# Kernel optimization log

Hardware: AMD Instinct MI355X
Metric: run time of the kernel (lower is better)

## Reference

```python
import jax, jax.numpy as jnp
import numpy as np

EPS = 1e-5
B, C, T = 128, 64, 1000          # batch, EEG channels, time samples
NCLU, HID, NOUT = 8, 512, 4      # clusters, head hidden dim, outputs (=feature_dim)


def _conv1d(x, w):
    # x: (N, Cin, T), w: (Cout, Cin, K), valid conv along time
    return jax.lax.conv_general_dilated(x, w, (1,), 'VALID',
                                        dimension_numbers=('NCH', 'OIH', 'NCH'))


def _bn(x, g, b, m, v):
    # eval-mode BatchNorm over channel dim of (N, C, T)
    return (x - m[None, :, None]) * (g / jnp.sqrt(v + EPS))[None, :, None] + b[None, :, None]


def _pool3(x):
    # maxpool kernel 3 stride 3 along time
    return jax.lax.reduce_window(x, -jnp.inf, jax.lax.max, (1, 1, 3), (1, 1, 3), 'VALID')


def setup_inputs() -> dict:
    key = jax.random.key(0)
    ks = jax.random.split(key, 12)
    def nrm(k, shape, fan):
        return jax.random.normal(k, shape, jnp.float32) / np.float32(np.sqrt(fan))
    inp = {
        'x': jax.random.normal(ks[0], (B, C, T), jnp.float32),
        'cluster_ids': jax.random.randint(ks[1], (B,), 0, NCLU, jnp.int32),
        # Deep4Net-style backbone params
        'w_time': nrm(ks[2], (25, 1, 10), 10),
        'b_time': jnp.zeros((25,), jnp.float32),
        'w_spat': nrm(ks[3], (25, 25, C), 25 * C),
        'w2': nrm(ks[4], (50, 25, 10), 250),
        'w3': nrm(ks[5], (100, 50, 10), 500),
        'w4': nrm(ks[6], (200, 100, 10), 1000),
        'w_cls': nrm(ks[7], (NOUT, 200, 7), 1400),
        'b_cls': jnp.zeros((NOUT,), jnp.float32),
        # per-cluster expert head params
        'hW1': nrm(ks[8], (NCLU, HID, NOUT), NOUT),
        'hb1': jnp.zeros((NCLU, HID), jnp.float32),
        'hW2': nrm(ks[9], (NCLU, NOUT, HID), HID),
        'hb2': jnp.zeros((NCLU, NOUT), jnp.float32),
        'hg': jnp.ones((NCLU, HID), jnp.float32),
        'hbe': jnp.zeros((NCLU, HID), jnp.float32),
        'hm': jnp.zeros((NCLU, HID), jnp.float32),
        'hv': jnp.ones((NCLU, HID), jnp.float32),
    }
    for i, c in zip((1, 2, 3, 4), (25, 50, 100, 200)):
        inp[f'g{i}'] = jnp.ones((c,), jnp.float32)
        inp[f'be{i}'] = jnp.zeros((c,), jnp.float32)
        inp[f'm{i}'] = jnp.zeros((c,), jnp.float32)
        inp[f'v{i}'] = jnp.ones((c,), jnp.float32)
    return inp


def reference(x, cluster_ids, w_time, b_time, w_spat, w2, w3, w4, w_cls, b_cls,
              hW1, hb1, hW2, hb2, hg, hbe, hm, hv,
              g1, be1, m1, v1, g2, be2, m2, v2, g3, be3, m3, v3, g4, be4, m4, v4):
    b_, c_, t_ = x.shape
    # conv_time: same 25 temporal filters applied per EEG channel -> (B, C, 25, T1)
    h = _conv1d(x.reshape(b_ * c_, 1, t_), w_time) + b_time[None, :, None]
    h = h.reshape(b_, c_, 25, -1)
    # conv_spat: collapse EEG channel axis -> (B, 25, T1)
    z = jnp.einsum('bcft,gfc->bgt', h, w_spat)
    z = _pool3(jax.nn.elu(_bn(z, g1, be1, m1, v1)))
    for w, g, be, m, v in ((w2, g2, be2, m2, v2), (w3, g3, be3, m3, v3), (w4, g4, be4, m4, v4)):
        z = _pool3(jax.nn.elu(_bn(_conv1d(z, w), g, be, m, v)))
    # final_conv_length='auto': classifier conv reduces time dim to 1 -> (B, NOUT)
    feats = (_conv1d(z, w_cls) + b_cls[None, :, None])[:, :, 0]
    # per-sample expert head routing (Linear -> BN(eval) -> ReLU -> [Dropout eval] -> Linear)
    h1 = jnp.einsum('bf,bhf->bh', feats, hW1[cluster_ids]) + hb1[cluster_ids]
    h1 = (h1 - hm[cluster_ids]) * (hg[cluster_ids] / jnp.sqrt(hv[cluster_ids] + EPS)) + hbe[cluster_ids]
    h1 = jax.nn.relu(h1)
    return jnp.einsum('bh,boh->bo', h1, hW2[cluster_ids]) + hb2[cluster_ids]
```

## Files before the change

kernel.cpp:

```cpp
#include <hip/hip_runtime.h>
#include <math.h>

#define EPS_BN 1e-5f

typedef __attribute__((ext_vector_type(8))) short short8;
typedef __attribute__((ext_vector_type(4))) float f32x4;
typedef __attribute__((ext_vector_type(4))) unsigned int uint4v;

__device__ __forceinline__ unsigned short f2bf(float f) {
    unsigned int u = __float_as_uint(f);
    u = (u + 0x7fffu + ((u >> 16) & 1u)) >> 16;
    return (unsigned short)u;
}
__device__ __forceinline__ float bf2f(unsigned short s) {
    return __uint_as_float(((unsigned int)s) << 16);
}
__device__ __forceinline__ float elu1(float y) { return y > 0.f ? y : expm1f(y); }
__device__ __forceinline__ float warp_sum(float v) {
    for (int off = 32; off > 0; off >>= 1) v += __shfl_down(v, off);
    return v;
}

#define UW1 0
#define UW2 20480
#define UW3 40960
#define UW4 122880
#define BB1 0
#define BB2 32
#define BB3 96
#define BB4 224
#define XTG_U 410496
#define Z1G_U 9192320
#define Z2G_U 10544000
#define Z3G_U 11420544
#define Z4G_BYTE 24372992

#define NPREP 1602
#define RS_ZB 36

__global__ __launch_bounds__(256) void kprep_tr(
    const float* __restrict__ x,
    const float* __restrict__ w_time, const float* __restrict__ b_time,
    const float* __restrict__ w_spat,
    const float* __restrict__ w2, const float* __restrict__ w3,
    const float* __restrict__ w4,
    const float* __restrict__ g1, const float* __restrict__ be1,
    const float* __restrict__ m1, const float* __restrict__ v1,
    const float* __restrict__ g2, const float* __restrict__ be2,
    const float* __restrict__ m2, const float* __restrict__ v2,
    const float* __restrict__ g3, const float* __restrict__ be3,
    const float* __restrict__ m3, const float* __restrict__ v3,
    const float* __restrict__ g4, const float* __restrict__ be4,
    const float* __restrict__ m4, const float* __restrict__ v4,
    unsigned short* __restrict__ wsz, float* __restrict__ biasf) {
    __shared__ float tr[64 * 65];
    if (blockIdx.x < NPREP) {
        int idx = blockIdx.x * 256 + threadIdx.x;
        if (idx < 20480) {
            int k = idx >> 11, g = (idx >> 6) & 31, c = idx & 63;
            float val = 0.f;
            if (g < 25) {
                float s = 0.f;
#pragma unroll
                for (int f = 0; f < 25; ++f)
                    s = fmaf(w_spat[g * 1600 + f * 64 + c], w_time[f * 10 + k], s);
                val = s * (g1[g] * rsqrtf(v1[g] + EPS_BN));
            }
            wsz[UW1 + idx] = f2bf(val);
        } else if (idx < 40960) {
            int j = idx - 20480;
            int k = j >> 11, g = (j >> 5) & 63, c = j & 31;
            float val = 0.f;
            if (g < 50 && c < 25)
                val = w2[(g * 25 + c) * 10 + k] * (g2[g] * rsqrtf(v2[g] + EPS_BN));
            wsz[UW2 + j] = f2bf(val);
        } else if (idx < 122880) {
            int j = idx - 40960;
            int k = j >> 13, g = (j >> 6) & 127, c = j & 63;
            float val = 0.f;
            if (g < 100 && c < 50)
                val = w3[(g * 50 + c) * 10 + k] * (g3[g] * rsqrtf(v3[g] + EPS_BN));
            wsz[UW3 + j] = f2bf(val);
        } else if (idx < 409600) {
            int j = idx - 122880;
            int k = j / 28672, r = j % 28672, g = r >> 7, c = r & 127;
            float val = 0.f;
            if (g < 200 && c < 100)
                val = w4[(g * 100 + c) * 10 + k] * (g4[g] * rsqrtf(v4[g] + EPS_BN));
            wsz[UW4 + j] = f2bf(val);
        } else if (idx < 410048) {
            int j = idx - 409600;
            if (j < 32) {
                int g = j; float val = 0.f;
                if (g < 25) {
                    float beff = 0.f;
                    for (int f = 0; f < 25; ++f) {
                        float a = 0.f;
                        for (int c = 0; c < 64; ++c) a += w_spat[g * 1600 + f * 64 + c];
                        beff = fmaf(a, b_time[f], beff);
                    }
                    float sc = g1[g] * rsqrtf(v1[g] + EPS_BN);
                    val = be1[g] - m1[g] * sc + beff * sc;
                }
                biasf[BB1 + g] = val;
            } else if (j < 96) {
                int g = j - 32; float val = 0.f;
                if (g < 50) { float sc = g2[g] * rsqrtf(v2[g] + EPS_BN); val = be2[g] - m2[g] * sc; }
                biasf[BB2 + g] = val;
            } else if (j < 224) {
                int g = j - 96; float val = 0.f;
                if (g < 100) { float sc = g3[g] * rsqrtf(v3[g] + EPS_BN); val = be3[g] - m3[g] * sc; }
                biasf[BB3 + g] = val;
            } else {
                int g = j - 224; float val = 0.f;
                if (g < 200) { float sc = g4[g] * rsqrtf(v4[g] + EPS_BN); val = be4[g] - m4[g] * sc; }
                biasf[BB4 + g] = val;
            }
        }
    } else {
        const int bid = blockIdx.x - NPREP;
        const int b = bid / 17, tile = bid % 17, t = threadIdx.x;
        const int t0 = tile * 64;
        const float* xb = x + b * 64000;
        for (int idx = t; idx < 1024; idx += 256) {
            int c = idx >> 4, q = idx & 15;
            int tg = t0 + 4 * q;
            float4 v = {0.f, 0.f, 0.f, 0.f};
            if (tg + 4 <= 1000) {
                v = *(const float4*)(xb + c * 1000 + tg);
            } else {
                float* pv = (float*)&v;
#pragma unroll
                for (int e = 0; e < 4; ++e)
                    if (tg + e < 1000) pv[e] = xb[c * 1000 + tg + e];
            }
            tr[c * 65 + 4 * q]     = v.x;
            tr[c * 65 + 4 * q + 1] = v.y;
            tr[c * 65 + 4 * q + 2] = v.z;
            tr[c * 65 + 4 * q + 3] = v.w;
        }
        __syncthreads();
        unsigned short* xTg = wsz + XTG_U;
        for (int idx = t; idx < 2048; idx += 256) {
            int tl = idx >> 5, cp = idx & 31;
            int tg = t0 + tl;
            unsigned int pk = 0u;
            if (tg < 1000)
                pk = (unsigned int)f2bf(tr[(2 * cp) * 65 + tl]) |
                     ((unsigned int)f2bf(tr[(2 * cp + 1) * 65 + tl]) << 16);
            if (tg < 1072)
                *(unsigned int*)&xTg[(b * 1072 + tg) * 64 + 2 * cp] = pk;
        }
    }
}

template<int CPAD, int RS, int SP, int TT, int TPC, int NCHUNK, int JMAX,
         int NTCH, int GPAD, int TPOOL, int GSTORE, int NGV, int OUT_RS,
         bool OUT_F32, int NW, int KPRE>
__device__ __forceinline__ void conv_core(
    const unsigned short* xT, const unsigned short* __restrict__ wpk,
    const float* __restrict__ bias,
    unsigned short* zout, float* zoutf, unsigned short* zb,
    int t, int jbeg, int jend, int t0b) {
    const int lane = t & 63;
    const int wv = __builtin_amdgcn_readfirstlane(t >> 6);
    const int lm = lane & 15, h8 = lane >> 4;
    const int gloc = lane & 31, hh = lane >> 5;
    unsigned short* zbw = zb + wv * (48 * RS_ZB);

    for (int job = jbeg + wv; job < jend; job += NW) {
        const int gbi = job / NTCH, tci = job % NTCH;
        const int tl0 = tci * (TT * 16) - t0b;
        const int po0 = tci * (NCHUNK * 16);

        f32x4 acc[TT][2];
#pragma unroll
        for (int i = 0; i < TT; ++i) {
            acc[i][0] = (f32x4){0.f, 0.f, 0.f, 0.f};
            acc[i][1] = (f32x4){0.f, 0.f, 0.f, 0.f};
        }

        const int abase = (tl0 + lm) * RS + h8 * 8;
        const unsigned short* wp = wpk + (gbi * 32 + lm) * CPAD + h8 * 8;
#pragma unroll
        for (int ph = 0; ph < 10 / KPRE; ++ph) {
            short8 w0r[KPRE][SP], w1r[KPRE][SP];
#pragma unroll
            for (int kk = 0; kk < KPRE; ++kk) {
                const int k = ph * KPRE + kk;
#pragma unroll
                for (int s = 0; s < SP; ++s) {
                    w0r[kk][s] = *(const short8*)(wp + k * (GPAD * CPAD) + s * 32);
                    w1r[kk][s] = *(const short8*)(wp + k * (GPAD * CPAD) + 16 * CPAD + s * 32);
                }
            }
#pragma unroll
            for (int kk = 0; kk < KPRE; ++kk) {
                const int k = ph * KPRE + kk;
#pragma unroll
                for (int s = 0; s < SP; ++s) {
#pragma unroll
                    for (int tt = 0; tt < TT; ++tt) {
                        short8 a = *(const short8*)&xT[abase + (tt * 16 + k) * RS + s * 32];
                        acc[tt][0] = __builtin_amdgcn_mfma_f32_16x16x32_bf16(
                            a, w0r[kk][s], acc[tt][0], 0, 0, 0);
                        acc[tt][1] = __builtin_amdgcn_mfma_f32_16x16x32_bf16(
                            a, w1r[kk][s], acc[tt][1], 0, 0, 0);
                    }
                }
            }
        }

        const float bv0 = bias[gbi * 32 + lm];
        const float bv1 = bias[gbi * 32 + 16 + lm];
#pragma unroll
        for (int ch = 0; ch < NCHUNK; ++ch) {
#pragma unroll
            for (int ti = 0; ti < TPC; ++ti) {
                int ttg = ch * TPC + ti;
#pragma unroll
                for (int r = 0; r < 4; ++r) {
                    float v0 = elu1(acc[ttg][0][r] + bv0);
                    float v1 = elu1(acc[ttg][1][r] + bv1);
                    int row = ti * 16 + 4 * h8 + r;
                    zbw[row * RS_ZB + lm] = f2bf(v0);
                    zbw[row * RS_ZB + 16 + lm] = f2bf(v1);
                }
            }
#pragma unroll
            for (int j = 0; j < JMAX; ++j) {
                int po = hh + 2 * j;
                if (3 * po + 2 < TPC * 16) {
                    float q0 = bf2f(zbw[(3 * po) * RS_ZB + gloc]);
                    float q1 = bf2f(zbw[(3 * po + 1) * RS_ZB + gloc]);
                    float q2 = bf2f(zbw[(3 * po + 2) * RS_ZB + gloc]);
                    float mx = fmaxf(q0, fmaxf(q1, q2));
                    int poa = po0 + ch * 16 + po;
                    int ga = gbi * 32 + gloc;
                    if (poa < TPOOL && ga < GSTORE) {
                        if constexpr (OUT_F32)
                            zoutf[poa * OUT_RS + ga] = mx;
                        else
                            zout[poa * OUT_RS + ga] =
                                (ga < NGV) ? f2bf(mx) : (unsigned short)0;
                    }
                }
            }
        }
    }
}

__global__ __launch_bounds__(64) void ks1(
    const unsigned short* __restrict__ wsu, const float* __restrict__ biasf,
    unsigned short* __restrict__ wsz) {
    __shared__ __align__(16) unsigned short xT[64 * 72];
    __shared__ __align__(16) unsigned short zb[48 * RS_ZB];
    const int b = blockIdx.x, tci = blockIdx.y, t = threadIdx.x;
    const int t0b = tci * 48;
    const unsigned short* xTg = wsz + XTG_U + (b * 1072 + t0b) * 64;
    for (int idx = t; idx < 64 * 8; idx += 64) {
        int r = idx >> 3, q = idx & 7;
        *(uint4v*)&xT[r * 72 + 8 * q] = *(const uint4v*)&xTg[r * 64 + 8 * q];
    }
    __syncthreads();
    conv_core<64, 72, 2, 3, 3, 1, 8, 21, 32, 330, 32, 25, 32, false, 1, 5>(
        xT, wsu + UW1, biasf + BB1, wsz + Z1G_U + b * 330 * 32, nullptr, zb,
        t, tci, tci + 1, t0b);
}

__global__ __launch_bounds__(64) void ks2(
    const unsigned short* __restrict__ wsu, const float* __restrict__ biasf,
    unsigned short* __restrict__ wsz) {
    __shared__ __align__(16) unsigned short xT[64 * 40];
    __shared__ __align__(16) unsigned short zb[48 * RS_ZB];
    const int b = blockIdx.x, job = blockIdx.y, t = threadIdx.x;
    const int t0b = (job % 7) * 48;
    const unsigned short* z1g = wsz + Z1G_U + b * 330 * 32;
    for (int idx = t; idx < 64 * 4; idx += 64) {
        int r = idx >> 2, q = idx & 3;
        uint4v v = {0u, 0u, 0u, 0u};
        if (t0b + r < 330) v = *(const uint4v*)&z1g[(t0b + r) * 32 + 8 * q];
        *(uint4v*)&xT[r * 40 + 8 * q] = v;
    }
    __syncthreads();
    conv_core<32, 40, 1, 3, 3, 1, 8, 7, 64, 107, 64, 50, 64, false, 1, 5>(
        xT, wsu + UW2, biasf + BB2, wsz + Z2G_U + b * 107 * 64, nullptr, zb,
        t, job, job + 1, t0b);
}

__global__ __launch_bounds__(64) void ks3(
    const unsigned short* __restrict__ wsu, const float* __restrict__ biasf,
    unsigned short* __restrict__ wsz) {
    __shared__ __align__(16) unsigned short z2t[64 * 72];
    __shared__ __align__(16) unsigned short zb[48 * RS_ZB];
    const int b = blockIdx.x, job = blockIdx.y, t = threadIdx.x;
    const int t0b = (job % 2) * 48;
    const unsigned short* z2g = wsz + Z2G_U + b * 107 * 64;
    for (int idx = t; idx < 64 * 8; idx += 64) {
        int r = idx >> 3, q = idx & 7;
        uint4v v = {0u, 0u, 0u, 0u};
        if (t0b + r < 107) v = *(const uint4v*)&z2g[(t0b + r) * 64 + 8 * q];
        *(uint4v*)&z2t[r * 72 + 8 * q] = v;
    }
    __syncthreads();
    conv_core<64, 72, 2, 3, 3, 1, 8, 2, 128, 32, 128, 100, 136, false, 1, 5>(
        z2t, wsu + UW3, biasf + BB3, wsz + Z3G_U + b * 44 * 136, nullptr, zb,
        t, job, job + 1, t0b);
}

__global__ __launch_bounds__(64) void ks4(
    const unsigned short* __restrict__ wsu, const float* __restrict__ biasf,
    unsigned short* __restrict__ wsz, float* __restrict__ z4g) {
    __shared__ __align__(16) unsigned short z3t[44 * 136];
    __shared__ __align__(16) unsigned short zb[48 * RS_ZB];
    const int b = blockIdx.x, gbi = blockIdx.y, t = threadIdx.x;
    const unsigned short* z3g = wsz + Z3G_U + b * 44 * 136;
    for (int idx = t; idx < 44 * 17; idx += 64) {
        int r = idx / 17, q = idx % 17;
        uint4v v = {0u, 0u, 0u, 0u};
        if (r < 32) v = *(const uint4v*)&z3g[r * 136 + 8 * q];
        *(uint4v*)&z3t[r * 136 + 8 * q] = v;
    }
    __syncthreads();
    conv_core<128, 136, 4, 2, 2, 1, 4, 1, 224, 7, 200, 200, 200, true, 1, 5>(
        z3t, wsu + UW4, biasf + BB4, nullptr, z4g + b * 1400, zb,
        t, gbi, gbi + 1, 0);
}

__global__ __launch_bounds__(256) void kh(
    const float* __restrict__ z4g,
    const float* __restrict__ w_cls, const float* __restrict__ b_cls,
    const int* __restrict__ cid,
    const float* __restrict__ hW1, const float* __restrict__ hb1,
    const float* __restrict__ hW2, const float* __restrict__ hb2,
    const float* __restrict__ hg, const float* __restrict__ hbe,
    const float* __restrict__ hm, const float* __restrict__ hv,
    float* __restrict__ out) {
    __shared__ float z4f[1400];
    __shared__ float feats[4];
    __shared__ float h1s[512];
    const int b = blockIdx.x, t = threadIdx.x;
    for (int i = t; i < 1400; i += 256) z4f[i] = z4g[b * 1400 + i];
    __syncthreads();

    const int wv = t >> 6, lane = t & 63;
    {
        float p = 0.f;
        for (int i = lane; i < 1400; i += 64) {
            int po = i / 200, g = i - po * 200;
            p = fmaf(z4f[i], w_cls[wv * 1400 + g * 7 + po], p);
        }
        p = warp_sum(p);
        if (lane == 0) feats[wv] = p + b_cls[wv];
    }
    __syncthreads();

    const int c = cid[b];
    const float f0 = feats[0], f1 = feats[1], f2 = feats[2], f3 = feats[3];
    for (int h = t; h < 512; h += 256) {
        const float* w1 = &hW1[(c * 512 + h) * 4];
        float v = f0 * w1[0] + f1 * w1[1] + f2 * w1[2] + f3 * w1[3] + hb1[c * 512 + h];
        float sc = hg[c * 512 + h] * rsqrtf(hv[c * 512 + h] + EPS_BN);
        v = (v - hm[c * 512 + h]) * sc + hbe[c * 512 + h];
        h1s[h] = fmaxf(v, 0.f);
    }
    __syncthreads();
    {
        float p = 0.f;
        for (int i = lane; i < 512; i += 64)
            p = fmaf(h1s[i], hW2[(c * 4 + wv) * 512 + i], p);
        p = warp_sum(p);
        if (lane == 0) out[b * 4 + wv] = p + hb2[c * 4 + wv];
    }
}

extern "C" void kernel_launch(void* const* d_in, const int* in_sizes, int n_in,
                              void* d_out, int out_size, void* d_ws, size_t ws_size,
                              hipStream_t stream) {
    const float* x      = (const float*)d_in[0];
    const int*   cid    = (const int*)d_in[1];
    const float* w_time = (const float*)d_in[2];
    const float* b_time = (const float*)d_in[3];
    const float* w_spat = (const float*)d_in[4];
    const float* w2     = (const float*)d_in[5];
    const float* w3     = (const float*)d_in[6];
    const float* w4     = (const float*)d_in[7];
    const float* w_cls  = (const float*)d_in[8];
    const float* b_cls  = (const float*)d_in[9];
    const float* hW1    = (const float*)d_in[10];
    const float* hb1    = (const float*)d_in[11];
    const float* hW2    = (const float*)d_in[12];
    const float* hb2    = (const float*)d_in[13];
    const float* hg     = (const float*)d_in[14];
    const float* hbe    = (const float*)d_in[15];
    const float* hm     = (const float*)d_in[16];
    const float* hv     = (const float*)d_in[17];
    const float* g1  = (const float*)d_in[18];
    const float* be1 = (const float*)d_in[19];
    const float* m1  = (const float*)d_in[20];
    const float* v1  = (const float*)d_in[21];
    const float* g2  = (const float*)d_in[22];
    const float* be2 = (const float*)d_in[23];
    const float* m2  = (const float*)d_in[24];
    const float* v2  = (const float*)d_in[25];
    const float* g3  = (const float*)d_in[26];
    const float* be3 = (const float*)d_in[27];
    const float* m3  = (const float*)d_in[28];
    const float* v3  = (const float*)d_in[29];
    const float* g4  = (const float*)d_in[30];
    const float* be4 = (const float*)d_in[31];
    const float* m4  = (const float*)d_in[32];
    const float* v4  = (const float*)d_in[33];

    unsigned short* wsz = (unsigned short*)d_ws;
    float* biasf = (float*)((char*)d_ws + 819200);
    float* z4g   = (float*)((char*)d_ws + Z4G_BYTE);
    float* out = (float*)d_out;

    kprep_tr<<<NPREP + 128 * 17, 256, 0, stream>>>(
        x, w_time, b_time, w_spat, w2, w3, w4,
        g1, be1, m1, v1, g2, be2, m2, v2, g3, be3, m3, v3, g4, be4, m4, v4,
        wsz, biasf);

    ks1<<<dim3(128, 21), 64, 0, stream>>>(wsz, biasf, wsz);
    ks2<<<dim3(128, 14), 64, 0, stream>>>(wsz, biasf, wsz);
    ks3<<<dim3(128, 8), 64, 0, stream>>>(wsz, biasf, wsz);
    ks4<<<dim3(128, 7), 64, 0, stream>>>(wsz, biasf, wsz, z4g);
    kh<<<128, 256, 0, stream>>>(z4g, w_cls, b_cls, cid, hW1, hb1, hW2, hb2,
                                hg, hbe, hm, hv, out);
}
```

Before: 102.4 us.

## Fuse input transpose into first conv and conv4 with head kernel

```diff
diff --git a/kernel.cpp b/kernel.cpp
--- a/kernel.cpp
+++ b/kernel.cpp
@@ -29,17 +29,13 @@
 #define BB2 32
 #define BB3 96
 #define BB4 224
-#define XTG_U 410496
 #define Z1G_U 9192320
 #define Z2G_U 10544000
 #define Z3G_U 11420544
-#define Z4G_BYTE 24372992
-
-#define NPREP 1602
+
 #define RS_ZB 36
 
-__global__ __launch_bounds__(256) void kprep_tr(
-    const float* __restrict__ x,
+__global__ __launch_bounds__(256) void kprep(
     const float* __restrict__ w_time, const float* __restrict__ b_time,
     const float* __restrict__ w_spat,
     const float* __restrict__ w2, const float* __restrict__ w3,
@@ -53,219 +49,195 @@
     const float* __restrict__ g4, const float* __restrict__ be4,
     const float* __restrict__ m4, const float* __restrict__ v4,
     unsigned short* __restrict__ wsz, float* __restrict__ biasf) {
-    __shared__ float tr[64 * 65];
-    if (blockIdx.x < NPREP) {
-        int idx = blockIdx.x * 256 + threadIdx.x;
-        if (idx < 20480) {
-            int k = idx >> 11, g = (idx >> 6) & 31, c = idx & 63;
-            float val = 0.f;
+    int idx = blockIdx.x * 256 + threadIdx.x;
+    if (idx < 20480) {
+        int k = idx >> 11, g = (idx >> 6) & 31, c = idx & 63;
+        float val = 0.f;
+        if (g < 25) {
+            float s = 0.f;
+#pragma unroll
+            for (int f = 0; f < 25; ++f)
+                s = fmaf(w_spat[g * 1600 + f * 64 + c], w_time[f * 10 + k], s);
+            val = s * (g1[g] * rsqrtf(v1[g] + EPS_BN));
+        }
+        wsz[UW1 + idx] = f2bf(val);
+    } else if (idx < 40960) {
+        int j = idx - 20480;
+        int k = j >> 11, g = (j >> 5) & 63, c = j & 31;
+        float val = 0.f;
+        if (g < 50 && c < 25)
+            val = w2[(g * 25 + c) * 10 + k] * (g2[g] * rsqrtf(v2[g] + EPS_BN));
+        wsz[UW2 + j] = f2bf(val);
+    } else if (idx < 122880) {
+        int j = idx - 40960;
+        int k = j >> 13, g = (j >> 6) & 127, c = j & 63;
+        float val = 0.f;
+        if (g < 100 && c < 50)
+            val = w3[(g * 50 + c) * 10 + k] * (g3[g] * rsqrtf(v3[g] + EPS_BN));
+        wsz[UW3 + j] = f2bf(val);
+    } else if (idx < 409600) {
+        int j = idx - 122880;
+        int k = j / 28672, r = j % 28672, g = r >> 7, c = r & 127;
+        float val = 0.f;
+        if (g < 200 && c < 100)
+            val = w4[(g * 100 + c) * 10 + k] * (g4[g] * rsqrtf(v4[g] + EPS_BN));
+        wsz[UW4 + j] = f2bf(val);
+    } else if (idx < 410048) {
+        int j = idx - 409600;
+        if (j < 32) {
+            int g = j; float val = 0.f;
             if (g < 25) {
-                float s = 0.f;
-#pragma unroll
-                for (int f = 0; f < 25; ++f)
-                    s = fmaf(w_spat[g * 1600 + f * 64 + c], w_time[f * 10 + k], s);
-                val = s * (g1[g] * rsqrtf(v1[g] + EPS_BN));
-            }
-            wsz[UW1 + idx] = f2bf(val);
-        } else if (idx < 40960) {
-            int j = idx - 20480;
-            int k = j >> 11, g = (j >> 5) & 63, c = j & 31;
-            float val = 0.f;
-            if (g < 50 && c < 25)
-                val = w2[(g * 25 + c) * 10 + k] * (g2[g] * rsqrtf(v2[g] + EPS_BN));
-            wsz[UW2 + j] = f2bf(val);
-        } else if (idx < 122880) {
-            int j = idx - 40960;
-            int k = j >> 13, g = (j >> 6) & 127, c = j & 63;
-            float val = 0.f;
-            if (g < 100 && c < 50)
-                val = w3[(g * 50 + c) * 10 + k] * (g3[g] * rsqrtf(v3[g] + EPS_BN));
-            wsz[UW3 + j] = f2bf(val);
-        } else if (idx < 409600) {
-            int j = idx - 122880;
-            int k = j / 28672, r = j % 28672, g = r >> 7, c = r & 127;
-            float val = 0.f;
-            if (g < 200 && c < 100)
-                val = w4[(g * 100 + c) * 10 + k] * (g4[g] * rsqrtf(v4[g] + EPS_BN));
-            wsz[UW4 + j] = f2bf(val);
-        } else if (idx < 410048) {
-            int j = idx - 409600;
-            if (j < 32) {
-                int g = j; float val = 0.f;
-                if (g < 25) {
-                    float beff = 0.f;
-                    for (int f = 0; f < 25; ++f) {
-                        float a = 0.f;
-                        for (int c = 0; c < 64; ++c) a += w_spat[g * 1600 + f * 64 + c];
-                        beff = fmaf(a, b_time[f], beff);
-                    }
-                    float sc = g1[g] * rsqrtf(v1[g] + EPS_BN);
-                    val = be1[g] - m1[g] * sc + beff * sc;
+                float beff = 0.f;
+                for (int f = 0; f < 25; ++f) {
+                    float a = 0.f;
+                    for (int c = 0; c < 64; ++c) a += w_spat[g * 1600 + f * 64 + c];
+                    beff = fmaf(a, b_time[f], beff);
                 }
-                biasf[BB1 + g] = val;
-            } else if (j < 96) {
-                int g = j - 32; float val = 0.f;
-                if (g < 50) { float sc = g2[g] * rsqrtf(v2[g] + EPS_BN); val = be2[g] - m2[g] * sc; }
-                biasf[BB2 + g] = val;
-            } else if (j < 224) {
-                int g = j - 96; float val = 0.f;
-                if (g < 100) { float sc = g3[g] * rsqrtf(v3[g] + EPS_BN); val = be3[g] - m3[g] * sc; }
-                biasf[BB3 + g] = val;
-            } else {
-                int g = j - 224; float val = 0.f;
-                if (g < 200) { float sc = g4[g] * rsqrtf(v4[g] + EPS_BN); val = be4[g] - m4[g] * sc; }
-                biasf[BB4 + g] = val;
-            }
-        }
-    } else {
-        const int bid = blockIdx.x - NPREP;
-        const int b = bid / 17, tile = bid % 17, t = threadIdx.x;
-        const int t0 = tile * 64;
-        const float* xb = x + b * 64000;
-        for (int idx = t; idx < 1024; idx += 256) {
-            int c = idx >> 4, q = idx & 15;
-            int tg = t0 + 4 * q;
-            float4 v = {0.f, 0.f, 0.f, 0.f};
-            if (tg + 4 <= 1000) {
-                v = *(const float4*)(xb + c * 1000 + tg);
-            } else {
-                float* pv = (float*)&v;
-#pragma unroll
-                for (int e = 0; e < 4; ++e)
-                    if (tg + e < 1000) pv[e] = xb[c * 1000 + tg + e];
-            }
-            tr[c * 65 + 4 * q]     = v.x;
-            tr[c * 65 + 4 * q + 1] = v.y;
-            tr[c * 65 + 4 * q + 2] = v.z;
-            tr[c * 65 + 4 * q + 3] = v.w;
-        }
-        __syncthreads();
-        unsigned short* xTg = wsz + XTG_U;
-        for (int idx = t; idx < 2048; idx += 256) {
-            int tl = idx >> 5, cp = idx & 31;
-            int tg = t0 + tl;
-            unsigned int pk = 0u;
-            if (tg < 1000)
-                pk = (unsigned int)f2bf(tr[(2 * cp) * 65 + tl]) |
-                     ((unsigned int)f2bf(tr[(2 * cp + 1) * 65 + tl]) << 16);
-            if (tg < 1072)
-                *(unsigned int*)&xTg[(b * 1072 + tg) * 64 + 2 * cp] = pk;
+                float sc = g1[g] * rsqrtf(v1[g] + EPS_BN);
+                val = be1[g] - m1[g] * sc + beff * sc;
+            }
+            biasf[BB1 + g] = val;
+        } else if (j < 96) {
+            int g = j - 32; float val = 0.f;
+            if (g < 50) { float sc = g2[g] * rsqrtf(v2[g] + EPS_BN); val = be2[g] - m2[g] * sc; }
+            biasf[BB2 + g] = val;
+        } else if (j < 224) {
+            int g = j - 96; float val = 0.f;
+            if (g < 100) { float sc = g3[g] * rsqrtf(v3[g] + EPS_BN); val = be3[g] - m3[g] * sc; }
+            biasf[BB3 + g] = val;
+        } else {
+            int g = j - 224; float val = 0.f;
+            if (g < 200) { float sc = g4[g] * rsqrtf(v4[g] + EPS_BN); val = be4[g] - m4[g] * sc; }
+            biasf[BB4 + g] = val;
         }
     }
 }
 
 template<int CPAD, int RS, int SP, int TT, int TPC, int NCHUNK, int JMAX,
-         int NTCH, int GPAD, int TPOOL, int GSTORE, int NGV, int OUT_RS,
-         bool OUT_F32, int NW, int KPRE>
-__device__ __forceinline__ void conv_core(
+         int GPAD, int TPOOL, int GSTORE, int NGV, int OUT_RS, bool OUT_F32,
+         int KPRE>
+__device__ __forceinline__ void conv_job(
     const unsigned short* xT, const unsigned short* __restrict__ wpk,
     const float* __restrict__ bias,
-    unsigned short* zout, float* zoutf, unsigned short* zb,
-    int t, int jbeg, int jend, int t0b) {
-    const int lane = t & 63;
-    const int wv = __builtin_amdgcn_readfirstlane(t >> 6);
+    unsigned short* zout, float* zoutf, unsigned short* zbw,
+    int lane, int gbi, int po0) {
     const int lm = lane & 15, h8 = lane >> 4;
     const int gloc = lane & 31, hh = lane >> 5;
-    unsigned short* zbw = zb + wv * (48 * RS_ZB);
-
-    for (int job = jbeg + wv; job < jend; job += NW) {
-        const int gbi = job / NTCH, tci = job % NTCH;
-        const int tl0 = tci * (TT * 16) - t0b;
-        const int po0 = tci * (NCHUNK * 16);
-
-        f32x4 acc[TT][2];
-#pragma unroll
-        for (int i = 0; i < TT; ++i) {
-            acc[i][0] = (f32x4){0.f, 0.f, 0.f, 0.f};
-            acc[i][1] = (f32x4){0.f, 0.f, 0.f, 0.f};
-        }
-
-        const int abase = (tl0 + lm) * RS + h8 * 8;
-        const unsigned short* wp = wpk + (gbi * 32 + lm) * CPAD + h8 * 8;
-#pragma unroll
-        for (int ph = 0; ph < 10 / KPRE; ++ph) {
-            short8 w0r[KPRE][SP], w1r[KPRE][SP];
-#pragma unroll
-            for (int kk = 0; kk < KPRE; ++kk) {
-                const int k = ph * KPRE + kk;
-#pragma unroll
-                for (int s = 0; s < SP; ++s) {
-                    w0r[kk][s] = *(const short8*)(wp + k * (GPAD * CPAD) + s * 32);
-                    w1r[kk][s] = *(const short8*)(wp + k * (GPAD * CPAD) + 16 * CPAD + s * 32);
+
+    f32x4 acc[TT][2];
+#pragma unroll
+    for (int i = 0; i < TT; ++i) {
+        acc[i][0] = (f32x4){0.f, 0.f, 0.f, 0.f};
+        acc[i][1] = (f32x4){0.f, 0.f, 0.f, 0.f};
+    }
+
+    const int abase = lm * RS + h8 * 8;
+    const unsigned short* wp = wpk + (gbi * 32 + lm) * CPAD + h8 * 8;
+#pragma unroll
+    for (int ph = 0; ph < 10 / KPRE; ++ph) {
+        short8 w0r[KPRE][SP], w1r[KPRE][SP];
+#pragma unroll
+        for (int kk = 0; kk < KPRE; ++kk) {
+            const int k = ph * KPRE + kk;
+#pragma unroll
+            for (int s = 0; s < SP; ++s) {
+                w0r[kk][s] = *(const short8*)(wp + k * (GPAD * CPAD) + s * 32);
+                w1r[kk][s] = *(const short8*)(wp + k * (GPAD * CPAD) + 16 * CPAD + s * 32);
+            }
+        }
+#pragma unroll
+        for (int kk = 0; kk < KPRE; ++kk) {
+            const int k = ph * KPRE + kk;
+#pragma unroll
+            for (int s = 0; s < SP; ++s) {
+#pragma unroll
+                for (int tt = 0; tt < TT; ++tt) {
+                    short8 a = *(const short8*)&xT[abase + (tt * 16 + k) * RS + s * 32];
+                    acc[tt][0] = __builtin_amdgcn_mfma_f32_16x16x32_bf16(
+                        a, w0r[kk][s], acc[tt][0], 0, 0, 0);
+                    acc[tt][1] = __builtin_amdgcn_mfma_f32_16x16x32_bf16(
+                        a, w1r[kk][s], acc[tt][1], 0, 0, 0);
                 }
             }
-#pragma unroll
-            for (int kk = 0; kk < KPRE; ++kk) {
-                const int k = ph * KPRE + kk;
-#pragma unroll
-                for (int s = 0; s < SP; ++s) {
-#pragma unroll
-                    for (int tt = 0; tt < TT; ++tt) {
-                        short8 a = *(const short8*)&xT[abase + (tt * 16 + k) * RS + s * 32];
-                        acc[tt][0] = __builtin_amdgcn_mfma_f32_16x16x32_bf16(
-                            a, w0r[kk][s], acc[tt][0], 0, 0, 0);
-                        acc[tt][1] = __builtin_amdgcn_mfma_f32_16x16x32_bf16(
-                            a, w1r[kk][s], acc[tt][1], 0, 0, 0);
-                    }
+        }
+    }
+
+    const float bv0 = bias[gbi * 32 + lm];
+    const float bv1 = bias[gbi * 32 + 16 + lm];
+#pragma unroll
+    for (int ch = 0; ch < NCHUNK; ++ch) {
+#pragma unroll
+        for (int ti = 0; ti < TPC; ++ti) {
+            int ttg = ch * TPC + ti;
+#pragma unroll
+            for (int r = 0; r < 4; ++r) {
+                float v0 = elu1(acc[ttg][0][r] + bv0);
+                float v1 = elu1(acc[ttg][1][r] + bv1);
+                int row = ti * 16 + 4 * h8 + r;
+                zbw[row * RS_ZB + lm] = f2bf(v0);
+                zbw[row * RS_ZB + 16 + lm] = f2bf(v1);
+            }
+        }
+#pragma unroll
+        for (int j = 0; j < JMAX; ++j) {
+            int po = hh + 2 * j;
+            if (3 * po + 2 < TPC * 16) {
+                float q0 = bf2f(zbw[(3 * po) * RS_ZB + gloc]);
+                float q1 = bf2f(zbw[(3 * po + 1) * RS_ZB + gloc]);
+                float q2 = bf2f(zbw[(3 * po + 2) * RS_ZB + gloc]);
+                float mx = fmaxf(q0, fmaxf(q1, q2));
+                int poa = po0 + ch * 16 + po;
+                int ga = gbi * 32 + gloc;
+                if (poa < TPOOL && ga < GSTORE) {
+                    if constexpr (OUT_F32)
+                        zoutf[poa * OUT_RS + ga] = mx;
+                    else
+                        zout[poa * OUT_RS + ga] =
+                            (ga < NGV) ? f2bf(mx) : (unsigned short)0;
                 }
             }
         }
-
-        const float bv0 = bias[gbi * 32 + lm];
-        const float bv1 = bias[gbi * 32 + 16 + lm];
-#pragma unroll
-        for (int ch = 0; ch < NCHUNK; ++ch) {
-#pragma unroll
-            for (int ti = 0; ti < TPC; ++ti) {
-                int ttg = ch * TPC + ti;
-#pragma unroll
-                for (int r = 0; r < 4; ++r) {
-                    float v0 = elu1(acc[ttg][0][r] + bv0);
-                    float v1 = elu1(acc[ttg][1][r] + bv1);
-                    int row = ti * 16 + 4 * h8 + r;
-                    zbw[row * RS_ZB + lm] = f2bf(v0);
-                    zbw[row * RS_ZB + 16 + lm] = f2bf(v1);
-                }
-            }
-#pragma unroll
-            for (int j = 0; j < JMAX; ++j) {
-                int po = hh + 2 * j;
-                if (3 * po + 2 < TPC * 16) {
-                    float q0 = bf2f(zbw[(3 * po) * RS_ZB + gloc]);
-                    float q1 = bf2f(zbw[(3 * po + 1) * RS_ZB + gloc]);
-                    float q2 = bf2f(zbw[(3 * po + 2) * RS_ZB + gloc]);
-                    float mx = fmaxf(q0, fmaxf(q1, q2));
-                    int poa = po0 + ch * 16 + po;
-                    int ga = gbi * 32 + gloc;
-                    if (poa < TPOOL && ga < GSTORE) {
-                        if constexpr (OUT_F32)
-                            zoutf[poa * OUT_RS + ga] = mx;
-                        else
-                            zout[poa * OUT_RS + ga] =
-                                (ga < NGV) ? f2bf(mx) : (unsigned short)0;
-                    }
-                }
-            }
-        }
     }
 }
 
 __global__ __launch_bounds__(64) void ks1(
+    const float* __restrict__ x,
     const unsigned short* __restrict__ wsu, const float* __restrict__ biasf,
     unsigned short* __restrict__ wsz) {
     __shared__ __align__(16) unsigned short xT[64 * 72];
     __shared__ __align__(16) unsigned short zb[48 * RS_ZB];
-    const int b = blockIdx.x, tci = blockIdx.y, t = threadIdx.x;
-    const int t0b = tci * 48;
-    const unsigned short* xTg = wsz + XTG_U + (b * 1072 + t0b) * 64;
-    for (int idx = t; idx < 64 * 8; idx += 64) {
-        int r = idx >> 3, q = idx & 7;
-        *(uint4v*)&xT[r * 72 + 8 * q] = *(const uint4v*)&xTg[r * 64 + 8 * q];
-    }
-    __syncthreads();
-    conv_core<64, 72, 2, 3, 3, 1, 8, 21, 32, 330, 32, 25, 32, false, 1, 5>(
-        xT, wsu + UW1, biasf + BB1, wsz + Z1G_U + b * 330 * 32, nullptr, zb,
-        t, tci, tci + 1, t0b);
+    const int b = blockIdx.x, tci = blockIdx.y, lane = threadIdx.x;
+    const int t0 = tci * 48;
+    const int cp = lane & 31, hf = lane >> 5;
+    const float* xr0 = x + b * 64000 + (2 * cp) * 1000;
+    const float* xr1 = xr0 + 1000;
+#pragma unroll
+    for (int q8 = 0; q8 < 8; ++q8) {
+        const int q = hf * 8 + q8;
+        const int tg = t0 + 4 * q;
+        float4 va = {0.f, 0.f, 0.f, 0.f}, vb = {0.f, 0.f, 0.f, 0.f};
+        if (tg + 4 <= 1000) {
+            va = *(const float4*)(xr0 + tg);
+            vb = *(const float4*)(xr1 + tg);
+        } else if (tg < 1000) {
+            float* pa = (float*)&va; float* pb = (float*)&vb;
+#pragma unroll
+            for (int e = 0; e < 4; ++e)
+                if (tg + e < 1000) { pa[e] = xr0[tg + e]; pb[e] = xr1[tg + e]; }
+        }
+        const float* pa = (const float*)&va;
+        const float* pb = (const float*)&vb;
+#pragma unroll
+        for (int e = 0; e < 4; ++e) {
+            unsigned int pk = (unsigned int)f2bf(pa[e]) |
+                              ((unsigned int)f2bf(pb[e]) << 16);
+            *(unsigned int*)&xT[(4 * q + e) * 72 + 2 * cp] = pk;
+        }
+    }
+    __syncthreads();
+    conv_job<64, 72, 2, 3, 3, 1, 8, 32, 330, 32, 25, 32, false, 5>(
+        xT, wsu + UW1, biasf + BB1,
+        wsz + Z1G_U + b * 330 * 32, nullptr, zb, lane, 0, tci * 16);
 }
 
 __global__ __launch_bounds__(64) void ks2(
@@ -273,19 +245,19 @@
     unsigned short* __restrict__ wsz) {
     __shared__ __align__(16) unsigned short xT[64 * 40];
     __shared__ __align__(16) unsigned short zb[48 * RS_ZB];
-    const int b = blockIdx.x, job = blockIdx.y, t = threadIdx.x;
-    const int t0b = (job % 7) * 48;
+    const int b = blockIdx.x, y = blockIdx.y, lane = threadIdx.x;
+    const int gbi = y / 7, tci = y % 7, t0b = tci * 48;
     const unsigned short* z1g = wsz + Z1G_U + b * 330 * 32;
-    for (int idx = t; idx < 64 * 4; idx += 64) {
+    for (int idx = lane; idx < 256; idx += 64) {
         int r = idx >> 2, q = idx & 3;
         uint4v v = {0u, 0u, 0u, 0u};
         if (t0b + r < 330) v = *(const uint4v*)&z1g[(t0b + r) * 32 + 8 * q];
         *(uint4v*)&xT[r * 40 + 8 * q] = v;
     }
     __syncthreads();
-    conv_core<32, 40, 1, 3, 3, 1, 8, 7, 64, 107, 64, 50, 64, false, 1, 5>(
-        xT, wsu + UW2, biasf + BB2, wsz + Z2G_U + b * 107 * 64, nullptr, zb,
-        t, job, job + 1, t0b);
+    conv_job<32, 40, 1, 3, 3, 1, 8, 64, 107, 64, 50, 64, false, 5>(
+        xT, wsu + UW2, biasf + BB2,
+        wsz + Z2G_U + b * 107 * 64, nullptr, zb, lane, gbi, tci * 16);
 }
 
 __global__ __launch_bounds__(64) void ks3(
@@ -293,42 +265,24 @@
     unsigned short* __restrict__ wsz) {
     __shared__ __align__(16) unsigned short z2t[64 * 72];
     __shared__ __align__(16) unsigned short zb[48 * RS_ZB];
-    const int b = blockIdx.x, job = blockIdx.y, t = threadIdx.x;
-    const int t0b = (job % 2) * 48;
+    const int b = blockIdx.x, y = blockIdx.y, lane = threadIdx.x;
+    const int gbi = y / 2, tci = y % 2, t0b = tci * 48;
     const unsigned short* z2g = wsz + Z2G_U + b * 107 * 64;
-    for (int idx = t; idx < 64 * 8; idx += 64) {
+    for (int idx = lane; idx < 512; idx += 64) {
         int r = idx >> 3, q = idx & 7;
         uint4v v = {0u, 0u, 0u, 0u};
         if (t0b + r < 107) v = *(const uint4v*)&z2g[(t0b + r) * 64 + 8 * q];
         *(uint4v*)&z2t[r * 72 + 8 * q] = v;
     }
     __syncthreads();
-    conv_core<64, 72, 2, 3, 3, 1, 8, 2, 128, 32, 128, 100, 136, false, 1, 5>(
-        z2t, wsu + UW3, biasf + BB3, wsz + Z3G_U + b * 44 * 136, nullptr, zb,
-        t, job, job + 1, t0b);
-}
-
-__global__ __launch_bounds__(64) void ks4(
+    conv_job<64, 72, 2, 3, 3, 1, 8, 128, 32, 128, 100, 136, false, 5>(
+        z2t, wsu + UW3, biasf + BB3,
+        wsz + Z3G_U + b * 44 * 136, nullptr, zb, lane, gbi, tci * 16);
+}
+
+__global__ __launch_bounds__(448) void ks4h(
     const unsigned short* __restrict__ wsu, const float* __restrict__ biasf,
-    unsigned short* __restrict__ wsz, float* __restrict__ z4g) {
-    __shared__ __align__(16) unsigned short z3t[44 * 136];
-    __shared__ __align__(16) unsigned short zb[48 * RS_ZB];
-    const int b = blockIdx.x, gbi = blockIdx.y, t = threadIdx.x;
-    const unsigned short* z3g = wsz + Z3G_U + b * 44 * 136;
-    for (int idx = t; idx < 44 * 17; idx += 64) {
-        int r = idx / 17, q = idx % 17;
-        uint4v v = {0u, 0u, 0u, 0u};
-        if (r < 32) v = *(const uint4v*)&z3g[r * 136 + 8 * q];
-        *(uint4v*)&z3t[r * 136 + 8 * q] = v;
-    }
-    __syncthreads();
-    conv_core<128, 136, 4, 2, 2, 1, 4, 1, 224, 7, 200, 200, 200, true, 1, 5>(
-        z3t, wsu + UW4, biasf + BB4, nullptr, z4g + b * 1400, zb,
-        t, gbi, gbi + 1, 0);
-}
-
-__global__ __launch_bounds__(256) void kh(
-    const float* __restrict__ z4g,
+    const unsigned short* __restrict__ wsz,
     const float* __restrict__ w_cls, const float* __restrict__ b_cls,
     const int* __restrict__ cid,
     const float* __restrict__ hW1, const float* __restrict__ hb1,
@@ -336,15 +290,28 @@
     const float* __restrict__ hg, const float* __restrict__ hbe,
     const float* __restrict__ hm, const float* __restrict__ hv,
     float* __restrict__ out) {
+    __shared__ __align__(16) unsigned short z3t[44 * 136];
+    __shared__ __align__(16) unsigned short zb[7 * 32 * RS_ZB];
     __shared__ float z4f[1400];
     __shared__ float feats[4];
     __shared__ float h1s[512];
     const int b = blockIdx.x, t = threadIdx.x;
-    for (int i = t; i < 1400; i += 256) z4f[i] = z4g[b * 1400 + i];
-    __syncthreads();
-
-    const int wv = t >> 6, lane = t & 63;
-    {
+    const int lane = t & 63, wv = t >> 6;
+    const unsigned short* z3g = wsz + Z3G_U + b * 44 * 136;
+    for (int idx = t; idx < 748; idx += 448) {
+        int r = idx / 17, q = idx % 17;
+        uint4v v = {0u, 0u, 0u, 0u};
+        if (r < 32) v = *(const uint4v*)&z3g[r * 136 + 8 * q];
+        *(uint4v*)&z3t[r * 136 + 8 * q] = v;
+    }
+    __syncthreads();
+
+    conv_job<128, 136, 4, 2, 2, 1, 4, 224, 7, 200, 200, 200, true, 5>(
+        z3t, wsu + UW4, biasf + BB4,
+        nullptr, z4f, zb + wv * (32 * RS_ZB), lane, wv, 0);
+    __syncthreads();
+
+    if (wv < 4) {
         float p = 0.f;
         for (int i = lane; i < 1400; i += 64) {
             int po = i / 200, g = i - po * 200;
@@ -357,7 +324,7 @@
 
     const int c = cid[b];
     const float f0 = feats[0], f1 = feats[1], f2 = feats[2], f3 = feats[3];
-    for (int h = t; h < 512; h += 256) {
+    for (int h = t; h < 512; h += 448) {
         const float* w1 = &hW1[(c * 512 + h) * 4];
         float v = f0 * w1[0] + f1 * w1[1] + f2 * w1[2] + f3 * w1[3] + hb1[c * 512 + h];
         float sc = hg[c * 512 + h] * rsqrtf(hv[c * 512 + h] + EPS_BN);
@@ -365,7 +332,7 @@
         h1s[h] = fmaxf(v, 0.f);
     }
     __syncthreads();
-    {
+    if (wv < 4) {
         float p = 0.f;
         for (int i = lane; i < 512; i += 64)
             p = fmaf(h1s[i], hW2[(c * 4 + wv) * 512 + i], p);
@@ -414,18 +381,16 @@
 
     unsigned short* wsz = (unsigned short*)d_ws;
     float* biasf = (float*)((char*)d_ws + 819200);
-    float* z4g   = (float*)((char*)d_ws + Z4G_BYTE);
     float* out = (float*)d_out;
 
-    kprep_tr<<<NPREP + 128 * 17, 256, 0, stream>>>(
-        x, w_time, b_time, w_spat, w2, w3, w4,
-        g1, be1, m1, v1, g2, be2, m2, v2, g3, be3, m3, v3, g4, be4, m4, v4,
-        wsz, biasf);
-
-    ks1<<<dim3(128, 21), 64, 0, stream>>>(wsz, biasf, wsz);
+    kprep<<<1602, 256, 0, stream>>>(w_time, b_time, w_spat, w2, w3, w4,
+                                    g1, be1, m1, v1, g2, be2, m2, v2,
+                                    g3, be3, m3, v3, g4, be4, m4, v4,
+                                    wsz, biasf);
+
+    ks1<<<dim3(128, 21), 64, 0, stream>>>(x, wsz, biasf, wsz);
     ks2<<<dim3(128, 14), 64, 0, stream>>>(wsz, biasf, wsz);
     ks3<<<dim3(128, 8), 64, 0, stream>>>(wsz, biasf, wsz);
-    ks4<<<dim3(128, 7), 64, 0, stream>>>(wsz, biasf, wsz, z4g);
-    kh<<<128, 256, 0, stream>>>(z4g, w_cls, b_cls, cid, hW1, hb1, hW2, hb2,
-                                hg, hbe, hm, hv, out);
-}
+    ks4h<<<128, 448, 0, stream>>>(wsz, biasf, wsz, w_cls, b_cls, cid,
+                                  hW1, hb1, hW2, hb2, hg, hbe, hm, hv, out);
+}
```

New measurement: 111.7 us. +9.1%, slower.
